# Performance work log

Measured on AMD Instinct MI355X. Metric: run time of the kernel, lower is better.

The kernel has to match this reference:

```python
import jax, jax.numpy as jnp
import numpy as np

N_NODES = 50000


def gcn_conv(x, src, dst, W, b, n_nodes):
    # PyG GCNConv: add self-loops, symmetric normalization D^-1/2 (A+I) D^-1/2 (x W) + b
    E = src.shape[0]
    deg = jax.ops.segment_sum(jnp.ones((E,), x.dtype), dst, num_segments=n_nodes) + 1.0
    dinv = jax.lax.rsqrt(deg)
    h = x @ W  # [N, H]
    norm = dinv[src] * dinv[dst]  # [E]
    agg = jax.ops.segment_sum(h[src] * norm[:, None], dst, num_segments=n_nodes)
    agg = agg + h * (dinv * dinv)[:, None]  # self-loop contribution
    return agg + b


def setup_inputs() -> dict:
    key = jax.random.key(0)
    ks = jax.random.split(key, 16)
    N, E, D, H, T, O = N_NODES, 800000, 128, 128, 2, 1
    x = jax.random.normal(ks[0], (N, D), jnp.float32)
    edge_index = jax.random.randint(ks[1], (2, E), 0, N, jnp.int32)
    edge_attrs = jax.random.uniform(ks[2], (T, E, 7), jnp.float32)
    s = lambda k, sh: jax.random.normal(k, sh, jnp.float32) * (1.0 / np.sqrt(sh[0]))
    return {
        "x": x, "edge_index": edge_index, "edge_attrs": edge_attrs,
        "W1": s(ks[3], (D, H)), "b1": jnp.zeros((H,), jnp.float32),
        "W2": s(ks[4], (H, H)), "b2": jnp.zeros((H,), jnp.float32),
        "W3": s(ks[5], (H, H)), "b3": jnp.zeros((H,), jnp.float32),
        "We": s(ks[6], (2 * H + 7, H)), "be": jnp.zeros((H,), jnp.float32),
        "Wg": s(ks[7], (H, O)), "bg": jnp.zeros((O,), jnp.float32),
    }


def reference(x, edge_index, edge_attrs, W1, b1, W2, b2, W3, b3, We, be, Wg, bg):
    src, dst = edge_index[0], edge_index[1]
    n = x.shape[0]
    outputs = []
    for t in range(edge_attrs.shape[0]):  # small fixed T, x evolves across iterations
        edge_attr = edge_attrs[t]
        x = jax.nn.relu(gcn_conv(x, src, dst, W1, b1, n))
        x = jax.nn.relu(gcn_conv(x, src, dst, W2, b2, n))
        x = jax.nn.relu(gcn_conv(x, src, dst, W3, b3, n))
        # gather-concat-MLP-mean per edge
        edge_features = jnp.concatenate([x[src], x[dst], edge_attr], axis=1)
        edge_output = jax.nn.relu(edge_features @ We + be)
        graph_features = jnp.mean(edge_output, axis=0, keepdims=True)  # [1, H]
        outputs.append(graph_features @ Wg + bg)
        W1 = W2  # no-op placeholder removed below
        W1 = W1  # keep W1 unchanged
    return jnp.concatenate(outputs, axis=0)  # [T, output_dim]
```

## Files before the change

### kernel.cpp

```cpp
#include <hip/hip_runtime.h>
#include <hip/hip_bf16.h>


typedef __attribute__((ext_vector_type(8))) short bf16x8;
typedef __attribute__((ext_vector_type(4))) float f32x4;
typedef __attribute__((ext_vector_type(2))) float f32x2;

__device__ __forceinline__ unsigned short f2bf(float f) {
    union { float f; unsigned int u; } v; v.f = f;
    unsigned int r = v.u + 0x7fffu + ((v.u >> 16) & 1u);
    return (unsigned short)(r >> 16);
}
__device__ __forceinline__ unsigned int pk2bf(float lo, float hi) {
    return (unsigned int)f2bf(lo) | ((unsigned int)f2bf(hi) << 16);
}
__device__ __forceinline__ unsigned char f2fp8(float f) {
    return (unsigned char)(__builtin_amdgcn_cvt_pk_fp8_f32(f, f, 0, false) & 0xff);
}
__device__ __forceinline__ void fp8x4(unsigned int u, float* o) {
    f32x2 lo = __builtin_amdgcn_cvt_pk_f32_fp8(u, false);
    f32x2 hi = __builtin_amdgcn_cvt_pk_f32_fp8(u, true);
    o[0] = lo[0]; o[1] = lo[1]; o[2] = hi[0]; o[3] = hi[1];
}
__device__ __forceinline__ f32x2 max0_2(f32x2 v) {
#if __has_builtin(__builtin_elementwise_max)
    return __builtin_elementwise_max(v, (f32x2){0.f, 0.f});
#else
    return (f32x2){fmaxf(v[0], 0.f), fmaxf(v[1], 0.f)};
#endif
}

__global__ void to_bf16(const float* __restrict__ in, unsigned short* __restrict__ out, int n4)
{
    int i = blockIdx.x * 256 + threadIdx.x;
    if (i < n4) {
        float4 v = ((const float4*)in)[i];
        ushort4 o;
        o.x = f2bf(v.x); o.y = f2bf(v.y); o.z = f2bf(v.z); o.w = f2bf(v.w);
        ((ushort4*)out)[i] = o;
    }
}

__global__ void transpose_w(
    const float* __restrict__ W1, const float* __restrict__ W2,
    const float* __restrict__ W3, const float* __restrict__ We,
    unsigned short* __restrict__ T1, unsigned short* __restrict__ T2,
    unsigned short* __restrict__ T3, unsigned short* __restrict__ Tuv)
{
    const float* src; unsigned short* dst;
    switch (blockIdx.y) {
        case 0:  src = W1;             dst = T1;               break;
        case 1:  src = W2;             dst = T2;               break;
        case 2:  src = W3;             dst = T3;               break;
        case 3:  src = We;             dst = Tuv;              break;
        case 4:  src = We + 128 * 128; dst = Tuv + 128 * 128;  break;
        default: src = W2;             dst = Tuv + 256 * 128;  break;
    }
    for (int i = blockIdx.x * 256 + threadIdx.x; i < 128 * 128; i += 256 * gridDim.x) {
        int k = i >> 7, c = i & 127;
        dst[c * 128 + k] = f2bf(src[i]);
    }
}

__global__ __launch_bounds__(256) void mfma_matmul(
    const unsigned short* __restrict__ X, const unsigned short* __restrict__ Wt,
    unsigned char* __restrict__ out, const float* __restrict__ scale, int n_rows)
{
    const int wave = threadIdx.x >> 6;
    const int lane = threadIdx.x & 63;
    const int m = lane & 15;
    const int q = lane >> 4;
    const int r = blockIdx.x * 64 + wave * 16 + m;
    const bool rv = r < n_rows;

    f32x4 acc[8];
    #pragma unroll
    for (int i = 0; i < 8; ++i) acc[i] = (f32x4){0.f, 0.f, 0.f, 0.f};

    #pragma unroll
    for (int k0 = 0; k0 < 128; k0 += 32) {
        bf16x8 a = {};
        if (rv) a = *(const bf16x8*)(X + (size_t)r * 128 + k0 + q * 8);
        #pragma unroll
        for (int ct = 0; ct < 8; ++ct) {
            bf16x8 b = *(const bf16x8*)(Wt + (ct * 16 + m) * 128 + k0 + q * 8);
            acc[ct] = __builtin_amdgcn_mfma_f32_16x16x32_bf16(a, b, acc[ct], 0, 0, 0);
        }
    }

    #pragma unroll
    for (int reg = 0; reg < 4; ++reg) {
        int gr = blockIdx.x * 64 + wave * 16 + q * 4 + reg;
        if (gr >= n_rows) continue;
        float s = scale[gr];
        #pragma unroll
        for (int ct = 0; ct < 8; ++ct)
            out[(size_t)gr * 128 + ct * 16 + m] = f2fp8(acc[ct][reg] * s);
    }
}

#define FPAD 136
#define GN 16
#define ICAP 64
#define ISTR 72
__global__ __launch_bounds__(256, 8) void fused_gm(
    const unsigned char* __restrict__ hs_in, const int* __restrict__ csr_src,
    const int* __restrict__ offs, const int* __restrict__ counts,
    const float* __restrict__ dinv, const float* __restrict__ bias,
    const unsigned short* __restrict__ Wt, int ncols, int uvcols,
    unsigned char* __restrict__ buv, unsigned char* __restrict__ bh, int n)
{
    __shared__ unsigned short xs[GN * FPAD];
    __shared__ int idxl[GN * ISTR];
    const int tid = threadIdx.x;
    const int row = tid >> 4;
    const int node = blockIdx.x * GN + row;
    const int lg = tid & 15;
    const int c8 = lg * 8;

    if (node < n) {
        const int off = offs[node];
        const int cnt = counts[node];
        const int cap = min(cnt, ICAP);

        for (int j = lg; j < cap; j += 16)
            idxl[row * ISTR + j] = csr_src[off + j];

        const uint2 sv = *(const uint2*)(hs_in + (size_t)node * 128 + c8);

        f32x2 a01 = {0.f, 0.f}, a23 = {0.f, 0.f}, a45 = {0.f, 0.f}, a67 = {0.f, 0.f};
        auto de8 = [&](uint2 v) {
            a01 += __builtin_amdgcn_cvt_pk_f32_fp8(v.x, false);
            a23 += __builtin_amdgcn_cvt_pk_f32_fp8(v.x, true);
            a45 += __builtin_amdgcn_cvt_pk_f32_fp8(v.y, false);
            a67 += __builtin_amdgcn_cvt_pk_f32_fp8(v.y, true);
        };
        uint2 A[4], B[4];
        auto LQ = [&](uint2* Q, int jb) {
            #pragma unroll
            for (int q = 0; q < 4; ++q)
                Q[q] = *(const uint2*)(hs_in + (size_t)idxl[row * ISTR + jb + q] * 128 + c8);
        };
        auto CONS = [&](uint2* Q) {
            #pragma unroll
            for (int q = 0; q < 4; ++q) de8(Q[q]);
        };

        int j = 0;
        if (cap >= 8) {
            LQ(A, 0); LQ(B, 4);
            de8(sv);
            j = 8;
            for (; j + 8 <= cap; j += 8) {
                CONS(A); LQ(A, j);
                CONS(B); LQ(B, j + 4);
            }
            CONS(A); CONS(B);
        } else if (cap >= 4) {
            LQ(A, 0);
            de8(sv);
            CONS(A);
            j = 4;
        } else {
            de8(sv);
        }
        if (j + 4 <= cap) {
            LQ(A, j); CONS(A); j += 4;
        }
        for (; j < cap; ++j)
            de8(*(const uint2*)(hs_in + (size_t)idxl[row * ISTR + j] * 128 + c8));
        for (; j < cnt; ++j)
            de8(*(const uint2*)(hs_in + (size_t)csr_src[off + j] * 128 + c8));

        const float dn = dinv[node];
        const float4 b0 = *(const float4*)(bias + c8);
        const float4 b1v = *(const float4*)(bias + c8 + 4);
        float r0 = fmaxf(fmaf(a01[0], dn, b0.x), 0.f);
        float r1 = fmaxf(fmaf(a01[1], dn, b0.y), 0.f);
        float r2 = fmaxf(fmaf(a23[0], dn, b0.z), 0.f);
        float r3 = fmaxf(fmaf(a23[1], dn, b0.w), 0.f);
        float r4 = fmaxf(fmaf(a45[0], dn, b1v.x), 0.f);
        float r5 = fmaxf(fmaf(a45[1], dn, b1v.y), 0.f);
        float r6 = fmaxf(fmaf(a67[0], dn, b1v.z), 0.f);
        float r7 = fmaxf(fmaf(a67[1], dn, b1v.w), 0.f);
        uint4 w;
        w.x = pk2bf(r0, r1); w.y = pk2bf(r2, r3);
        w.z = pk2bf(r4, r5); w.w = pk2bf(r6, r7);
        *(uint4*)&xs[row * FPAD + c8] = w;
    }
    __syncthreads();

    const int wave = tid >> 6;
    const int lane = tid & 63;
    const int m = lane & 15;
    const int q = lane >> 4;
    const int nct = ncols >> 4;
    const int per = nct >> 2;
    const int ct0 = wave * per;

    for (int ci = 0; ci < per; ++ci) {
        const int ct = ct0 + ci;
        f32x4 acc = (f32x4){0.f, 0.f, 0.f, 0.f};
        #pragma unroll
        for (int k0 = 0; k0 < 128; k0 += 32) {
            bf16x8 a = *(const bf16x8*)&xs[m * FPAD + k0 + q * 8];
            bf16x8 b = *(const bf16x8*)(Wt + (size_t)(ct * 16 + m) * 128 + k0 + q * 8);
            acc = __builtin_amdgcn_mfma_f32_16x16x32_bf16(a, b, acc, 0, 0, 0);
        }
        const int col = ct * 16 + m;
        #pragma unroll
        for (int reg = 0; reg < 4; ++reg) {
            int nd = blockIdx.x * GN + q * 4 + reg;
            if (nd >= n) continue;
            if (col < uvcols)
                buv[(size_t)nd * 256 + col] = f2fp8(acc[reg]);
            else
                bh[(size_t)nd * 128 + col - uvcols] = f2fp8(acc[reg] * dinv[nd]);
        }
    }
}

#define EM_CHUNK 256
__global__ __launch_bounds__(256) void edge_mlp(
    const unsigned char* __restrict__ uv, const int* __restrict__ src,
    const int* __restrict__ dst, const float* __restrict__ ea,
    const float* __restrict__ We_e, const float* __restrict__ be,
    const float* __restrict__ Wg, float* __restrict__ acc, int E)
{
    const int tid  = threadIdx.x;
    const int lane = tid & 31;
    const int g    = tid >> 5;
    const int c4   = lane * 4;

    __shared__ float eas[EM_CHUNK * 7];
    __shared__ int   ss[EM_CHUNK];
    __shared__ int   ds[EM_CHUNK];
    __shared__ float red[256];

    f32x2 wlo[7], whi[7];
    #pragma unroll
    for (int i = 0; i < 7; ++i) {
        float4 wv = *(const float4*)(We_e + i * 128 + c4);
        wlo[i] = (f32x2){wv.x, wv.y};
        whi[i] = (f32x2){wv.z, wv.w};
    }
    const float4 bev = *(const float4*)(be + c4);
    const f32x2 be01 = (f32x2){bev.x, bev.y};
    const f32x2 be23 = (f32x2){bev.z, bev.w};
    const float4 wg4 = *(const float4*)(Wg + c4);

    f32x2 part01 = {0.f, 0.f}, part23 = {0.f, 0.f};

    for (int base = blockIdx.x * EM_CHUNK; base < E; base += gridDim.x * EM_CHUNK) {
        const int nch = min(EM_CHUNK, E - base);
        for (int i = tid; i < nch * 7; i += 256)
            eas[i] = ea[(size_t)base * 7 + i];
        for (int i = tid; i < nch; i += 256) {
            ss[i] = src[base + i];
            ds[i] = dst[base + i];
        }
        __syncthreads();

        auto ev = [&](int j) {
            unsigned int us = *(const unsigned int*)(uv + (size_t)ss[j] * 256 + c4);
            unsigned int vs = *(const unsigned int*)(uv + (size_t)ds[j] * 256 + 128 + c4);
            f32x2 u01 = __builtin_amdgcn_cvt_pk_f32_fp8(us, false);
            f32x2 u23 = __builtin_amdgcn_cvt_pk_f32_fp8(us, true);
            f32x2 v01 = __builtin_amdgcn_cvt_pk_f32_fp8(vs, false);
            f32x2 v23 = __builtin_amdgcn_cvt_pk_f32_fp8(vs, true);
            f32x2 val01 = u01 + v01 + be01;
            f32x2 val23 = u23 + v23 + be23;
            const float* eav = &eas[j * 7];
            #pragma unroll
            for (int i = 0; i < 7; ++i) {
                f32x2 e2 = (f32x2){eav[i], eav[i]};
                val01 += e2 * wlo[i];
                val23 += e2 * whi[i];
            }
            part01 += max0_2(val01);
            part23 += max0_2(val23);
        };

        int j = g;
        for (; j + 32 <= nch; j += 32) {
            ev(j); ev(j + 8); ev(j + 16); ev(j + 24);
        }
        for (; j < nch; j += 8)
            ev(j);
        __syncthreads();
    }

    float p = part01[0] * wg4.x + part01[1] * wg4.y + part23[0] * wg4.z + part23[1] * wg4.w;
    red[tid] = p;
    __syncthreads();
    for (int s = 128; s > 0; s >>= 1) {
        if (tid < s) red[tid] += red[tid + s];
        __syncthreads();
    }
    if (tid == 0) atomicAdd(acc, red[0]);
}

__global__ void count_edges(const int* __restrict__ dst, int* __restrict__ counts, int E)
{
    int e = blockIdx.x * 256 + threadIdx.x;
    if (e < E) atomicAdd(&counts[dst[e]], 1);
}

__global__ void compute_dinv(const int* __restrict__ counts, float* __restrict__ dinv, int n)
{
    int i = blockIdx.x * 256 + threadIdx.x;
    if (i < n) dinv[i] = rsqrtf((float)counts[i] + 1.0f);
}

__global__ void scan1(const int* __restrict__ counts, int* __restrict__ scanned,
                      int* __restrict__ btot, int n)
{
    __shared__ int sh[256];
    int i = blockIdx.x * 256 + threadIdx.x;
    int v = (i < n) ? counts[i] : 0;
    sh[threadIdx.x] = v;
    __syncthreads();
    for (int off = 1; off < 256; off <<= 1) {
        int t = (threadIdx.x >= off) ? sh[threadIdx.x - off] : 0;
        __syncthreads();
        sh[threadIdx.x] += t;
        __syncthreads();
    }
    if (i < n) scanned[i] = sh[threadIdx.x] - v;
    if (threadIdx.x == 255) btot[blockIdx.x] = sh[255];
}

__global__ void scan2(int* __restrict__ btot, int nb)
{
    __shared__ int sh[256];
    int v = (threadIdx.x < nb) ? btot[threadIdx.x] : 0;
    sh[threadIdx.x] = v;
    __syncthreads();
    for (int off = 1; off < 256; off <<= 1) {
        int t = (threadIdx.x >= off) ? sh[threadIdx.x - off] : 0;
        __syncthreads();
        sh[threadIdx.x] += t;
        __syncthreads();
    }
    if (threadIdx.x < nb) btot[threadIdx.x] = sh[threadIdx.x] - v;
}

__global__ void scan3(const int* __restrict__ scanned, const int* __restrict__ btot,
                      int* __restrict__ offs, int* __restrict__ cursor, int n)
{
    int i = blockIdx.x * 256 + threadIdx.x;
    if (i < n) {
        int o = scanned[i] + btot[blockIdx.x];
        offs[i] = o;
        cursor[i] = o;
    }
}

__global__ void fill_csr(const int* __restrict__ src, const int* __restrict__ dst,
                         int* __restrict__ cursor, int* __restrict__ csr_src, int E)
{
    int e = blockIdx.x * 256 + threadIdx.x;
    if (e < E) {
        int slot = atomicAdd(&cursor[dst[e]], 1);
        csr_src[slot] = src[e];
    }
}

__global__ void write_out(const float* __restrict__ acc, const float* __restrict__ bg,
                          float* __restrict__ out, float invE, int T)
{
    int t = threadIdx.x;
    if (t < T) out[t] = acc[t] * invE + bg[0];
}


extern "C" void kernel_launch(void* const* d_in, const int* in_sizes, int n_in,
                              void* d_out, int out_size, void* d_ws, size_t ws_size,
                              hipStream_t stream)
{
    const float* x   = (const float*)d_in[0];
    const int*  eidx = (const int*)d_in[1];
    const float* ea  = (const float*)d_in[2];
    const float* W1  = (const float*)d_in[3];
    const float* b1  = (const float*)d_in[4];
    const float* W2  = (const float*)d_in[5];
    const float* b2  = (const float*)d_in[6];
    const float* W3  = (const float*)d_in[7];
    const float* b3  = (const float*)d_in[8];
    const float* We  = (const float*)d_in[9];
    const float* be  = (const float*)d_in[10];
    const float* Wg  = (const float*)d_in[11];
    const float* bg  = (const float*)d_in[12];

    const int N = in_sizes[0] / 128;
    const int E = in_sizes[1] / 2;
    const int T = in_sizes[2] / (E * 7);
    const int* src = eidx;
    const int* dst = eidx + E;

    char* wsp = (char*)d_ws;
    auto alloc = [&](size_t bytes) -> char* {
        char* p = wsp;
        wsp += (bytes + 255) / 256 * 256;
        return p;
    };
    int*   counts  = (int*)alloc((size_t)N * 4);
    int*   offs    = (int*)alloc((size_t)N * 4);
    int*   cursor  = (int*)alloc((size_t)N * 4);
    int*   scanned = (int*)alloc((size_t)N * 4);
    int*   btot    = (int*)alloc(1024);
    int*   csr_src = (int*)alloc((size_t)E * 4);
    float* dinv    = (float*)alloc((size_t)N * 4);
    float* acc     = (float*)alloc(256);
    unsigned short* X0  = (unsigned short*)alloc((size_t)N * 128 * 2);
    unsigned char*  Bh0 = (unsigned char*)alloc((size_t)N * 128);
    unsigned char*  Bh1 = (unsigned char*)alloc((size_t)N * 128);
    unsigned char*  Buv = (unsigned char*)alloc((size_t)N * 256);
    unsigned short* T1  = (unsigned short*)alloc(128 * 128 * 2);
    unsigned short* T2  = (unsigned short*)alloc(128 * 128 * 2);
    unsigned short* T3  = (unsigned short*)alloc(128 * 128 * 2);
    unsigned short* Tuv = (unsigned short*)alloc(384 * 128 * 2);

    hipMemsetAsync(counts, 0, (size_t)N * 4, stream);
    hipMemsetAsync(acc, 0, (size_t)T * 4, stream);

    to_bf16<<<(N * 128 / 4 + 255) / 256, 256, 0, stream>>>(x, X0, N * 128 / 4);
    transpose_w<<<dim3(8, 6), 256, 0, stream>>>(W1, W2, W3, We, T1, T2, T3, Tuv);

    count_edges<<<(E + 255) / 256, 256, 0, stream>>>(dst, counts, E);
    compute_dinv<<<(N + 255) / 256, 256, 0, stream>>>(counts, dinv, N);
    const int nb = (N + 255) / 256;
    scan1<<<nb, 256, 0, stream>>>(counts, scanned, btot, N);
    scan2<<<1, 256, 0, stream>>>(btot, nb);
    scan3<<<nb, 256, 0, stream>>>(scanned, btot, offs, cursor, N);
    fill_csr<<<(E + 255) / 256, 256, 0, stream>>>(src, dst, cursor, csr_src, E);

    const int mmb = (N + 63) / 64;
    const int fgb = (N + GN - 1) / GN;
    const int emb = (E + EM_CHUNK - 1) / EM_CHUNK;

    unsigned char* hcur = Bh0;
    unsigned char* hnxt = Bh1;

    for (int t = 0; t < T; ++t) {
        if (t == 0) {
            mfma_matmul<<<mmb, 256, 0, stream>>>(X0, T1, hcur, dinv, N);
        }
        fused_gm<<<fgb, 256, 0, stream>>>(hcur, csr_src, offs, counts, dinv, b1,
                                          T2, 128, 0, Buv, hnxt, N);
        { unsigned char* tmp = hcur; hcur = hnxt; hnxt = tmp; }
        fused_gm<<<fgb, 256, 0, stream>>>(hcur, csr_src, offs, counts, dinv, b2,
                                          T3, 128, 0, Buv, hnxt, N);
        { unsigned char* tmp = hcur; hcur = hnxt; hnxt = tmp; }
        bool last = (t == T - 1);
        fused_gm<<<fgb, 256, 0, stream>>>(hcur, csr_src, offs, counts, dinv, b3,
                                          Tuv, last ? 256 : 384, 256, Buv, hnxt, N);
        if (!last) { unsigned char* tmp = hcur; hcur = hnxt; hnxt = tmp; }

        edge_mlp<<<emb, 256, 0, stream>>>(Buv, src, dst, ea + (size_t)t * E * 7,
                                          We + 256 * 128, be, Wg, acc + t, E);
    }
    write_out<<<1, 64, 0, stream>>>(acc, bg, (float*)d_out, 1.0f / (float)E, T);
}
```

Before: 564.6 us.

## Co-schedule edge MLP with next GCN layer and build CSR without cursor atomics

Between timesteps, the edge MLP for step t now runs inside one combined kernel together with the first GCN layer of step t+1. Blocks are interleaved by a role index, so the two independent workloads share the GPU and save a launch boundary. CSR construction records each edge's rank during degree counting, and a partitioned fill then writes slots directly, replacing the second atomic pass and the cursor array. The combined kernel uses a shared LDS buffer and the higher launch-bounds occupancy hint, which may restrict registers for the edge body. The fill also rereads all edges in eight partitions.

```diff
diff --git a/kernel.cpp b/kernel.cpp
--- a/kernel.cpp
+++ b/kernel.cpp
@@ -16,11 +16,6 @@
 }
 __device__ __forceinline__ unsigned char f2fp8(float f) {
     return (unsigned char)(__builtin_amdgcn_cvt_pk_fp8_f32(f, f, 0, false) & 0xff);
-}
-__device__ __forceinline__ void fp8x4(unsigned int u, float* o) {
-    f32x2 lo = __builtin_amdgcn_cvt_pk_f32_fp8(u, false);
-    f32x2 hi = __builtin_amdgcn_cvt_pk_f32_fp8(u, true);
-    o[0] = lo[0]; o[1] = lo[1]; o[2] = hi[0]; o[3] = hi[1];
 }
 __device__ __forceinline__ f32x2 max0_2(f32x2 v) {
 #if __has_builtin(__builtin_elementwise_max)
@@ -103,18 +98,23 @@
 #define GN 16
 #define ICAP 64
 #define ISTR 72
-__global__ __launch_bounds__(256, 8) void fused_gm(
+#define FUSED_LDS (GN * FPAD * 2 + GN * ISTR * 4)
+#define EDGE_LDS  10240
+#define EM_CHUNK 256
+
+__device__ __forceinline__ void fused_body(
+    int bx, char* smem,
     const unsigned char* __restrict__ hs_in, const int* __restrict__ csr_src,
     const int* __restrict__ offs, const int* __restrict__ counts,
     const float* __restrict__ dinv, const float* __restrict__ bias,
     const unsigned short* __restrict__ Wt, int ncols, int uvcols,
     unsigned char* __restrict__ buv, unsigned char* __restrict__ bh, int n)
 {
-    __shared__ unsigned short xs[GN * FPAD];
-    __shared__ int idxl[GN * ISTR];
+    unsigned short* xs = (unsigned short*)smem;
+    int* idxl = (int*)(smem + GN * FPAD * 2);
     const int tid = threadIdx.x;
     const int row = tid >> 4;
-    const int node = blockIdx.x * GN + row;
+    const int node = bx * GN + row;
     const int lg = tid & 15;
     const int c8 = lg * 8;
 
@@ -210,7 +210,7 @@
         const int col = ct * 16 + m;
         #pragma unroll
         for (int reg = 0; reg < 4; ++reg) {
-            int nd = blockIdx.x * GN + q * 4 + reg;
+            int nd = bx * GN + q * 4 + reg;
             if (nd >= n) continue;
             if (col < uvcols)
                 buv[(size_t)nd * 256 + col] = f2fp8(acc[reg]);
@@ -220,22 +220,22 @@
     }
 }
 
-#define EM_CHUNK 256
-__global__ __launch_bounds__(256) void edge_mlp(
+__device__ __forceinline__ void edge_body(
+    int bx, int nbx, char* smem,
     const unsigned char* __restrict__ uv, const int* __restrict__ src,
     const int* __restrict__ dst, const float* __restrict__ ea,
     const float* __restrict__ We_e, const float* __restrict__ be,
     const float* __restrict__ Wg, float* __restrict__ acc, int E)
 {
+    float* eas = (float*)smem;
+    int*   ss  = (int*)(smem + 7168);
+    int*   ds  = (int*)(smem + 8192);
+    float* red = (float*)(smem + 9216);
+
     const int tid  = threadIdx.x;
     const int lane = tid & 31;
     const int g    = tid >> 5;
     const int c4   = lane * 4;
-
-    __shared__ float eas[EM_CHUNK * 7];
-    __shared__ int   ss[EM_CHUNK];
-    __shared__ int   ds[EM_CHUNK];
-    __shared__ float red[256];
 
     f32x2 wlo[7], whi[7];
     #pragma unroll
@@ -251,7 +251,7 @@
 
     f32x2 part01 = {0.f, 0.f}, part23 = {0.f, 0.f};
 
-    for (int base = blockIdx.x * EM_CHUNK; base < E; base += gridDim.x * EM_CHUNK) {
+    for (int base = bx * EM_CHUNK; base < E; base += nbx * EM_CHUNK) {
         const int nch = min(EM_CHUNK, E - base);
         for (int i = tid; i < nch * 7; i += 256)
             eas[i] = ea[(size_t)base * 7 + i];
@@ -300,10 +300,69 @@
     if (tid == 0) atomicAdd(acc, red[0]);
 }
 
-__global__ void count_edges(const int* __restrict__ dst, int* __restrict__ counts, int E)
+__global__ __launch_bounds__(256, 8) void fused_gm(
+    const unsigned char* __restrict__ hs_in, const int* __restrict__ csr_src,
+    const int* __restrict__ offs, const int* __restrict__ counts,
+    const float* __restrict__ dinv, const float* __restrict__ bias,
+    const unsigned short* __restrict__ Wt, int ncols, int uvcols,
+    unsigned char* __restrict__ buv, unsigned char* __restrict__ bh, int n)
+{
+    __shared__ __align__(16) char smem[FUSED_LDS];
+    fused_body(blockIdx.x, smem, hs_in, csr_src, offs, counts, dinv, bias,
+               Wt, ncols, uvcols, buv, bh, n);
+}
+
+__global__ __launch_bounds__(256) void edge_mlp(
+    const unsigned char* __restrict__ uv, const int* __restrict__ src,
+    const int* __restrict__ dst, const float* __restrict__ ea,
+    const float* __restrict__ We_e, const float* __restrict__ be,
+    const float* __restrict__ Wg, float* __restrict__ acc, int E)
+{
+    __shared__ __align__(16) char smem[EDGE_LDS];
+    edge_body(blockIdx.x, gridDim.x, smem, uv, src, dst, ea, We_e, be, Wg, acc, E);
+}
+
+__global__ __launch_bounds__(256, 8) void fused_gm_edge(
+    int nf,
+    const unsigned char* __restrict__ hs_in, const int* __restrict__ csr_src,
+    const int* __restrict__ offs, const int* __restrict__ counts,
+    const float* __restrict__ dinv, const float* __restrict__ bias,
+    const unsigned short* __restrict__ Wt, int ncols, int uvcols,
+    unsigned char* __restrict__ buv, unsigned char* __restrict__ bh, int n,
+    int ne,
+    const unsigned char* __restrict__ uv, const int* __restrict__ src,
+    const int* __restrict__ dst, const float* __restrict__ ea,
+    const float* __restrict__ We_e, const float* __restrict__ be,
+    const float* __restrict__ Wg, float* __restrict__ acc, int E)
+{
+    __shared__ __align__(16) char smem[EDGE_LDS];
+    const int bid = blockIdx.x;
+    const int nmin = (nf < ne) ? nf : ne;
+    const int nch8 = nmin >> 3;
+    const int inter = nch8 * 16;
+    int role, idx;
+    if (bid < inter) {
+        int gg = bid >> 4, s = bid & 15;
+        role = s >> 3;
+        idx = gg * 8 + (s & 7);
+    } else {
+        int r = bid - inter;
+        int fleft = nf - nch8 * 8;
+        if (r < fleft) { role = 0; idx = nch8 * 8 + r; }
+        else           { role = 1; idx = nch8 * 8 + (r - fleft); }
+    }
+    if (role == 0)
+        fused_body(idx, smem, hs_in, csr_src, offs, counts, dinv, bias,
+                   Wt, ncols, uvcols, buv, bh, n);
+    else
+        edge_body(idx, ne, smem, uv, src, dst, ea, We_e, be, Wg, acc, E);
+}
+
+__global__ void count_edges(const int* __restrict__ dst, int* __restrict__ counts,
+                            int* __restrict__ rank, int E)
 {
     int e = blockIdx.x * 256 + threadIdx.x;
-    if (e < E) atomicAdd(&counts[dst[e]], 1);
+    if (e < E) rank[e] = atomicAdd(&counts[dst[e]], 1);
 }
 
 __global__ void compute_dinv(const int* __restrict__ counts, float* __restrict__ dinv, int n)
@@ -346,23 +405,26 @@
 }
 
 __global__ void scan3(const int* __restrict__ scanned, const int* __restrict__ btot,
-                      int* __restrict__ offs, int* __restrict__ cursor, int n)
+                      int* __restrict__ offs, int n)
 {
     int i = blockIdx.x * 256 + threadIdx.x;
-    if (i < n) {
-        int o = scanned[i] + btot[blockIdx.x];
-        offs[i] = o;
-        cursor[i] = o;
-    }
-}
-
-__global__ void fill_csr(const int* __restrict__ src, const int* __restrict__ dst,
-                         int* __restrict__ cursor, int* __restrict__ csr_src, int E)
-{
-    int e = blockIdx.x * 256 + threadIdx.x;
-    if (e < E) {
-        int slot = atomicAdd(&cursor[dst[e]], 1);
-        csr_src[slot] = src[e];
+    if (i < n) offs[i] = scanned[i] + btot[blockIdx.x];
+}
+
+__global__ void fill_csr2(const int* __restrict__ src, const int* __restrict__ dst,
+                          const int* __restrict__ rank, const int* __restrict__ offs,
+                          int* __restrict__ csr_src, int E, int n)
+{
+    const int g8 = blockIdx.x & 7;
+    const int b8 = blockIdx.x >> 3;
+    const int nb8 = gridDim.x >> 3;
+    const int chunk = (n + 7) >> 3;
+    const int lo = g8 * chunk;
+    const int hi = min(n, lo + chunk);
+    for (int e = b8 * 256 + threadIdx.x; e < E; e += nb8 * 256) {
+        int d = dst[e];
+        if (d >= lo && d < hi)
+            csr_src[offs[d] + rank[e]] = src[e];
     }
 }
 
@@ -406,9 +468,9 @@
     };
     int*   counts  = (int*)alloc((size_t)N * 4);
     int*   offs    = (int*)alloc((size_t)N * 4);
-    int*   cursor  = (int*)alloc((size_t)N * 4);
     int*   scanned = (int*)alloc((size_t)N * 4);
     int*   btot    = (int*)alloc(1024);
+    int*   rank    = (int*)alloc((size_t)E * 4);
     int*   csr_src = (int*)alloc((size_t)E * 4);
     float* dinv    = (float*)alloc((size_t)N * 4);
     float* acc     = (float*)alloc(256);
@@ -427,13 +489,13 @@
     to_bf16<<<(N * 128 / 4 + 255) / 256, 256, 0, stream>>>(x, X0, N * 128 / 4);
     transpose_w<<<dim3(8, 6), 256, 0, stream>>>(W1, W2, W3, We, T1, T2, T3, Tuv);
 
-    count_edges<<<(E + 255) / 256, 256, 0, stream>>>(dst, counts, E);
+    count_edges<<<(E + 255) / 256, 256, 0, stream>>>(dst, counts, rank, E);
     compute_dinv<<<(N + 255) / 256, 256, 0, stream>>>(counts, dinv, N);
     const int nb = (N + 255) / 256;
     scan1<<<nb, 256, 0, stream>>>(counts, scanned, btot, N);
     scan2<<<1, 256, 0, stream>>>(btot, nb);
-    scan3<<<nb, 256, 0, stream>>>(scanned, btot, offs, cursor, N);
-    fill_csr<<<(E + 255) / 256, 256, 0, stream>>>(src, dst, cursor, csr_src, E);
+    scan3<<<nb, 256, 0, stream>>>(scanned, btot, offs, N);
+    fill_csr2<<<2048, 256, 0, stream>>>(src, dst, rank, offs, csr_src, E, N);
 
     const int mmb = (N + 63) / 64;
     const int fgb = (N + GN - 1) / GN;
@@ -441,24 +503,34 @@
 
     unsigned char* hcur = Bh0;
     unsigned char* hnxt = Bh1;
+    auto swap = [&]() { unsigned char* tmp = hcur; hcur = hnxt; hnxt = tmp; };
+
+    mfma_matmul<<<mmb, 256, 0, stream>>>(X0, T1, hcur, dinv, N);
+    fused_gm<<<fgb, 256, 0, stream>>>(hcur, csr_src, offs, counts, dinv, b1,
+                                      T2, 128, 0, Buv, hnxt, N);
+    swap();
+    fused_gm<<<fgb, 256, 0, stream>>>(hcur, csr_src, offs, counts, dinv, b2,
+                                      T3, 128, 0, Buv, hnxt, N);
+    swap();
 
     for (int t = 0; t < T; ++t) {
-        if (t == 0) {
-            mfma_matmul<<<mmb, 256, 0, stream>>>(X0, T1, hcur, dinv, N);
-        }
-        fused_gm<<<fgb, 256, 0, stream>>>(hcur, csr_src, offs, counts, dinv, b1,
-                                          T2, 128, 0, Buv, hnxt, N);
-        { unsigned char* tmp = hcur; hcur = hnxt; hnxt = tmp; }
-        fused_gm<<<fgb, 256, 0, stream>>>(hcur, csr_src, offs, counts, dinv, b2,
-                                          T3, 128, 0, Buv, hnxt, N);
-        { unsigned char* tmp = hcur; hcur = hnxt; hnxt = tmp; }
-        bool last = (t == T - 1);
+        const bool last = (t == T - 1);
         fused_gm<<<fgb, 256, 0, stream>>>(hcur, csr_src, offs, counts, dinv, b3,
                                           Tuv, last ? 256 : 384, 256, Buv, hnxt, N);
-        if (!last) { unsigned char* tmp = hcur; hcur = hnxt; hnxt = tmp; }
-
-        edge_mlp<<<emb, 256, 0, stream>>>(Buv, src, dst, ea + (size_t)t * E * 7,
-                                          We + 256 * 128, be, Wg, acc + t, E);
+        if (last) {
+            edge_mlp<<<emb, 256, 0, stream>>>(Buv, src, dst, ea + (size_t)t * E * 7,
+                                              We + 256 * 128, be, Wg, acc + t, E);
+        } else {
+            swap();
+            fused_gm_edge<<<fgb + emb, 256, 0, stream>>>(
+                fgb, hcur, csr_src, offs, counts, dinv, b1, T2, 128, 0, Buv, hnxt, N,
+                emb, Buv, src, dst, ea + (size_t)t * E * 7,
+                We + 256 * 128, be, Wg, acc + t, E);
+            swap();
+            fused_gm<<<fgb, 256, 0, stream>>>(hcur, csr_src, offs, counts, dinv, b2,
+                                              T3, 128, 0, Buv, hnxt, N);
+            swap();
+        }
     }
     write_out<<<1, 64, 0, stream>>>(acc, bg, (float*)d_out, 1.0f / (float)E, T);
 }
```

New measurement: 542.0 us. 1.04x faster.
